# Kernel tuning notes

Measured on AMD Instinct MI355X. Metric: run time of the kernel, lower is better.

## Reference

```python
import math
import jax, jax.numpy as jnp
import numpy as np

B, T, C, H = 1, 512, 768, 12
D = C // H           # head_dim = 64
TOPK_GATE = 128      # config.hoa_top_k
EPS = 1e-5


def _ln(x, w, b):
    m = x.mean(-1, keepdims=True)
    v = ((x - m) ** 2).mean(-1, keepdims=True)
    return (x - m) * jax.lax.rsqrt(v + EPS) * w + b


def _split_heads(x):  # (B,T,C) -> (B,H,T,D)
    return x.reshape(B, T, H, D).transpose(0, 2, 1, 3)


def _sdpa_causal(q, k, v):  # (B,H,T,D) each
    s = jnp.einsum('bhtd,bhsd->bhts', q, k) / math.sqrt(D)
    t = jnp.arange(T)
    s = jnp.where(t[:, None] >= t[None, :], s, -jnp.inf)
    return jnp.einsum('bhts,bhsd->bhtd', jax.nn.softmax(s, axis=-1), v)


def _gather_time(t4, idx):
    # t4: (B,H,T,D), idx: (B,H,T,k) -> (B,H,T,k,D)
    k = idx.shape[-1]
    src = jnp.broadcast_to(t4[:, :, :, None, :], (B, H, T, k, D))
    ind = jnp.broadcast_to(idx[..., None], (B, H, T, k, D))
    return jnp.take_along_axis(src, ind, axis=2)


def _hoa(x, wq, wk1, wk2, wv1, wv2, wo):
    # order-3 higher-order attention with per-branch top-k gathered keys/values
    k_keep = max(1, math.ceil(T ** (2.0 / 3.0)))  # 64 for T=512
    scale = D ** -0.5
    q = _split_heads(x @ wq)
    tar = jnp.arange(T)
    causal_ok = tar[:, None] >= tar[None, :]          # allowed positions
    j = jnp.arange(k_keep)
    # torch code pads short rows (t+1 < k_keep) by repeating the last valid topk idx
    clip = jnp.minimum(j[None, :], tar[:, None])      # (T, k_keep)
    gK, gV = [], []
    for wk, wv in ((wk1, wv1), (wk2, wv2)):
        K = _split_heads(x @ wk)
        V = _split_heads(x @ wv)
        logits = jnp.einsum('bhtd,bhsd->bhts', q, K) * scale
        logits = jnp.where(causal_ok[None, None], logits, -jnp.inf)
        idx = jax.lax.top_k(logits, k_keep)[1]        # (B,H,T,k_keep)
        idx = jnp.take_along_axis(idx, jnp.broadcast_to(clip, idx.shape), axis=-1)
        gK.append(_gather_time(K, idx))
        gV.append(_gather_time(V, idx))
    A = jnp.einsum('bhid,bhijd,bhikd->bhijk', q, gK[0], gK[1]) * scale
    alpha = jax.nn.softmax(A, axis=-1)                # softmax over LAST axis only (as torch)
    out = jnp.einsum('bhijk,bhijd,bhikd->bhid', alpha, gV[0], gV[1])
    return out.transpose(0, 2, 1, 3).reshape(B, T, C) @ wo


def _forward(x, ln1_w, ln1_b, qkv_w, qkv_b, atto_w, atto_b,
             lnh_w, lnh_b, hq_w, hk1_w, hk2_w, hv1_w, hv2_w, ho_w,
             gate_w, gate_b, ln2_w, ln2_b, fc_w, fc_b, pr_w, pr_b):
    # causal self-attention branch
    h = _ln(x, ln1_w, ln1_b)
    qkv = h @ qkv_w + qkv_b
    q, k, v = jnp.split(qkv, 3, axis=-1)
    y = _sdpa_causal(_split_heads(q), _split_heads(k), _split_heads(v))
    y = y.transpose(0, 2, 1, 3).reshape(B, T, C) @ atto_w + atto_b
    x = x + y
    # higher-order attention branch with gated top-k token mask
    hoa_in = _ln(x, lnh_w, lnh_b)
    hoa_out = _hoa(hoa_in, hq_w, hk1_w, hk2_w, hv1_w, hv2_w, ho_w)
    scores = (hoa_in @ gate_w + gate_b)[..., 0]       # (B,T)
    kk = min(TOPK_GATE, T)
    idx = jax.lax.top_k(scores, kk)[1]                # (B,kk)
    mask = jnp.zeros((B, T), x.dtype).at[jnp.arange(B)[:, None], idx].set(1.0)
    x = x + hoa_out * mask[..., None]
    # MLP
    h2 = _ln(x, ln2_w, ln2_b)
    x = x + (jax.nn.gelu(h2 @ fc_w + fc_b, approximate=False) @ pr_w + pr_b)
    return x


def setup_inputs() -> dict:
    key = jax.random.key(0)
    ks = jax.random.split(key, 13)
    def w(k, shape):
        return jax.random.normal(k, shape, jnp.float32) * 0.02
    return dict(
        x=jax.random.normal(ks[0], (B, T, C), jnp.float32),
        ln1_w=jnp.ones(C, jnp.float32), ln1_b=jnp.zeros(C, jnp.float32),
        qkv_w=w(ks[1], (C, 3 * C)), qkv_b=jnp.zeros(3 * C, jnp.float32),
        atto_w=w(ks[2], (C, C)), atto_b=jnp.zeros(C, jnp.float32),
        lnh_w=jnp.ones(C, jnp.float32), lnh_b=jnp.zeros(C, jnp.float32),
        hq_w=w(ks[3], (C, C)), hk1_w=w(ks[4], (C, C)), hk2_w=w(ks[5], (C, C)),
        hv1_w=w(ks[6], (C, C)), hv2_w=w(ks[7], (C, C)), ho_w=w(ks[8], (C, C)),
        gate_w=w(ks[9], (C, 1)), gate_b=jnp.zeros(1, jnp.float32),
        ln2_w=jnp.ones(C, jnp.float32), ln2_b=jnp.zeros(C, jnp.float32),
        fc_w=w(ks[10], (C, 4 * C)), fc_b=jnp.zeros(4 * C, jnp.float32),
        pr_w=w(ks[11], (4 * C, C)), pr_b=jnp.zeros(C, jnp.float32),
    )


def reference(x, ln1_w, ln1_b, qkv_w, qkv_b, atto_w, atto_b,
              lnh_w, lnh_b, hq_w, hk1_w, hk2_w, hv1_w, hv2_w, ho_w,
              gate_w, gate_b, ln2_w, ln2_b, fc_w, fc_b, pr_w, pr_b):
    return _forward(x, ln1_w, ln1_b, qkv_w, qkv_b, atto_w, atto_b,
                    lnh_w, lnh_b, hq_w, hk1_w, hk2_w, hv1_w, hv2_w, ho_w,
                    gate_w, gate_b, ln2_w, ln2_b, fc_w, fc_b, pr_w, pr_b)
```

## Files before the change

kernel.cpp:

```cpp
#include <hip/hip_runtime.h>
#include <hip/hip_bf16.h>
#include <math.h>

#define TT 512
#define CC 768
#define HH 12
#define DD 64
#define KKEEP 64
#define TOPG 128
#define NTCE (TT * CC)
#define NPAIR 36

typedef __attribute__((ext_vector_type(8))) short bf16x8;
typedef __attribute__((ext_vector_type(8))) unsigned short ushort8v;
typedef __attribute__((ext_vector_type(4))) float f32x4;
typedef unsigned long long u64;

__device__ __forceinline__ float block_sum(float v, float* red) {
#pragma unroll
  for (int off = 32; off; off >>= 1) v += __shfl_xor(v, off);
  __syncthreads();
  if ((threadIdx.x & 63) == 0) red[threadIdx.x >> 6] = v;
  __syncthreads();
  return red[0] + red[1] + red[2] + red[3];
}

__device__ __forceinline__ unsigned short f32_to_bf16_rne(float f) {
  unsigned u = __float_as_uint(f);
  unsigned r = (u + 0x7FFFu + ((u >> 16) & 1u)) >> 16;
  return (unsigned short)r;
}
__device__ __forceinline__ float bf16_to_f32(unsigned short h) {
  return __uint_as_float(((unsigned)h) << 16);
}
__device__ __forceinline__ void split2(float x, unsigned short& h, unsigned short& l) {
  h = f32_to_bf16_rne(x);
  l = f32_to_bf16_rne(x - bf16_to_f32(h));
}
__device__ __forceinline__ int swz(int row, int k) {
  return row * 64 + ((((k >> 3) ^ (row & 7))) << 3) + (k & 7);
}

struct WSplitArgs {
  const float* src[10];
  unsigned short* hi[10];
  unsigned short* lo[10];
  int K[10], N[10], tstart[10];
};

__global__ __launch_bounds__(256) void wsplitT_kernel(WSplitArgs a) {
  __shared__ float tile_[64][65];
  int t = blockIdx.x;
  int wsel = 0;
#pragma unroll
  for (int i = 1; i < 10; i++)
    if (t >= a.tstart[i]) wsel = i;
  int local = t - a.tstart[wsel];
  int K = a.K[wsel], N = a.N[wsel];
  int ntn = N >> 6;
  int bn = local % ntn, bk = local / ntn;
  int tid = threadIdx.x, r = tid >> 2, cq = tid & 3;
  const float* src = a.src[wsel] + (size_t)(bk * 64 + r) * N + bn * 64 + cq * 16;
#pragma unroll
  for (int f = 0; f < 4; f++) {
    float4 v = *(const float4*)(src + f * 4);
    tile_[r][cq * 16 + f * 4 + 0] = v.x;
    tile_[r][cq * 16 + f * 4 + 1] = v.y;
    tile_[r][cq * 16 + f * 4 + 2] = v.z;
    tile_[r][cq * 16 + f * 4 + 3] = v.w;
  }
  __syncthreads();
  size_t dst = (size_t)(bn * 64 + r) * K + bk * 64 + cq * 16;
  unsigned short hv[16], lv[16];
#pragma unroll
  for (int i = 0; i < 16; i++) split2(tile_[cq * 16 + i][r], hv[i], lv[i]);
  *(ushort8v*)&a.hi[wsel][dst] = *(const ushort8v*)&hv[0];
  *(ushort8v*)&a.hi[wsel][dst + 8] = *(const ushort8v*)&hv[8];
  *(ushort8v*)&a.lo[wsel][dst] = *(const ushort8v*)&lv[0];
  *(ushort8v*)&a.lo[wsel][dst + 8] = *(const ushort8v*)&lv[8];
}

__global__ void ln_bf_kernel(const float* __restrict__ x, const float* __restrict__ w,
                             const float* __restrict__ b,
                             unsigned short* __restrict__ ohi, unsigned short* __restrict__ olo,
                             const float* __restrict__ gw, const float* __restrict__ gb,
                             float* __restrict__ gscore) {
  int t = blockIdx.x, tid = threadIdx.x;
  __shared__ float red[4];
  float ls = 0.f;
  for (int c = tid; c < CC; c += 256) ls += x[t * CC + c];
  float mean = block_sum(ls, red) * (1.f / CC);
  float lv = 0.f;
  for (int c = tid; c < CC; c += 256) { float d = x[t * CC + c] - mean; lv += d * d; }
  float var = block_sum(lv, red) * (1.f / CC);
  float rs = rsqrtf(var + 1e-5f);
  float gpart = 0.f;
  for (int c = tid; c < CC; c += 256) {
    float val = (x[t * CC + c] - mean) * rs * w[c] + b[c];
    if (gscore) gpart += val * gw[c];
    unsigned short hb, lb;
    split2(val, hb, lb);
    ohi[t * CC + c] = hb;
    olo[t * CC + c] = lb;
  }
  if (gscore) {
    float s = block_sum(gpart, red);
    if (tid == 0) gscore[t] = s + gb[0];
  }
}

__global__ __launch_bounds__(256) void gemm_bf(
    const unsigned short* __restrict__ Ah, const unsigned short* __restrict__ Al,
    const unsigned short* __restrict__ Bh, const unsigned short* __restrict__ Bl,
    const float* __restrict__ bias, float* __restrict__ Cf,
    unsigned short* __restrict__ Chi, unsigned short* __restrict__ Clo,
    int M, int N, int K, int act, int seg, const float* __restrict__ res,
    const float* __restrict__ rowmask, float* __restrict__ part) {
  __shared__ unsigned short AsH[64 * 64], AsL[64 * 64], BsH[64 * 64], BsL[64 * 64];
  int tid = threadIdx.x, lane = tid & 63, wave = tid >> 6;
  int wr = wave >> 1, wc = wave & 1, lr = lane & 15;
  int ksub = (lane >> 4) * 8;
  int n0 = blockIdx.x * 64, m0 = blockIdx.y * 64;
  int lrow = tid >> 2, lq = tid & 3;
  int kchunk = K / gridDim.z;
  int kstart = blockIdx.z * kchunk;

  f32x4 acc[2][2];
#pragma unroll
  for (int i = 0; i < 2; i++)
#pragma unroll
    for (int j = 0; j < 2; j++) acc[i][j] = (f32x4){0.f, 0.f, 0.f, 0.f};

  for (int k0 = kstart; k0 < kstart + kchunk; k0 += 64) {
    size_t aoff = (size_t)(m0 + lrow) * K + k0 + lq * 16;
    size_t boff = (size_t)(n0 + lrow) * K + k0 + lq * 16;
    int d0 = lrow * 64 + (((lq * 2) ^ (lrow & 7)) << 3);
    int d1 = lrow * 64 + (((lq * 2 + 1) ^ (lrow & 7)) << 3);
    *(ushort8v*)&AsH[d0] = *(const ushort8v*)&Ah[aoff];
    *(ushort8v*)&AsH[d1] = *(const ushort8v*)&Ah[aoff + 8];
    *(ushort8v*)&AsL[d0] = *(const ushort8v*)&Al[aoff];
    *(ushort8v*)&AsL[d1] = *(const ushort8v*)&Al[aoff + 8];
    *(ushort8v*)&BsH[d0] = *(const ushort8v*)&Bh[boff];
    *(ushort8v*)&BsH[d1] = *(const ushort8v*)&Bh[boff + 8];
    *(ushort8v*)&BsL[d0] = *(const ushort8v*)&Bl[boff];
    *(ushort8v*)&BsL[d1] = *(const ushort8v*)&Bl[boff + 8];
    __syncthreads();
#pragma unroll
    for (int kb = 0; kb < 2; kb++) {
      int kloc = kb * 32 + ksub;
      bf16x8 ah[2], al[2], bh[2], bl[2];
#pragma unroll
      for (int i = 0; i < 2; i++) {
        int m = wr * 32 + i * 16 + lr;
        int off = swz(m, kloc);
        ah[i] = *(const bf16x8*)&AsH[off];
        al[i] = *(const bf16x8*)&AsL[off];
      }
#pragma unroll
      for (int j = 0; j < 2; j++) {
        int n = wc * 32 + j * 16 + lr;
        int off = swz(n, kloc);
        bh[j] = *(const bf16x8*)&BsH[off];
        bl[j] = *(const bf16x8*)&BsL[off];
      }
#pragma unroll
      for (int i = 0; i < 2; i++)
#pragma unroll
        for (int j = 0; j < 2; j++) {
          acc[i][j] = __builtin_amdgcn_mfma_f32_16x16x32_bf16(ah[i], bh[j], acc[i][j], 0, 0, 0);
          acc[i][j] = __builtin_amdgcn_mfma_f32_16x16x32_bf16(ah[i], bl[j], acc[i][j], 0, 0, 0);
          acc[i][j] = __builtin_amdgcn_mfma_f32_16x16x32_bf16(al[i], bh[j], acc[i][j], 0, 0, 0);
        }
    }
    __syncthreads();
  }
  if (part) {
    float* pb = part + (size_t)blockIdx.z * M * N;
#pragma unroll
    for (int i = 0; i < 2; i++)
#pragma unroll
      for (int j = 0; j < 2; j++) {
        int col = n0 + wc * 32 + j * 16 + lr;
#pragma unroll
        for (int q = 0; q < 4; q++) {
          int row = m0 + wr * 32 + i * 16 + (lane >> 4) * 4 + q;
          pb[(size_t)row * N + col] = acc[i][j][q];
        }
      }
    return;
  }
#pragma unroll
  for (int i = 0; i < 2; i++)
#pragma unroll
    for (int j = 0; j < 2; j++) {
      int col = n0 + wc * 32 + j * 16 + lr;
      float bv = bias ? bias[col] : 0.f;
#pragma unroll
      for (int q = 0; q < 4; q++) {
        int row = m0 + wr * 32 + i * 16 + (lane >> 4) * 4 + q;
        float v = acc[i][j][q] + bv;
        if (act == 1) v = 0.5f * v * (1.f + erff(v * 0.70710678118654752f));
        if (rowmask) v *= rowmask[row];
        if (Cf) {
          size_t off = seg ? (size_t)(col / CC) * NTCE + (size_t)row * CC + (col % CC)
                           : (size_t)row * N + col;
          if (res) v += res[off];
          Cf[off] = v;
        }
        if (Chi) {
          size_t o2 = (size_t)row * N + col;
          unsigned short hb, lb;
          split2(v, hb, lb);
          Chi[o2] = hb;
          Clo[o2] = lb;
        }
      }
    }
}

__global__ __launch_bounds__(256) void gemm_combine_kernel(
    const float* __restrict__ part, int ksplit, int M, int N,
    const float* __restrict__ bias, float* __restrict__ Cf,
    unsigned short* __restrict__ Chi, unsigned short* __restrict__ Clo,
    int act, const float* __restrict__ res, const float* __restrict__ rowmask) {
  int i = blockIdx.x * 256 + threadIdx.x;
  if (i >= M * N) return;
  int row = i / N, col = i - row * N;
  float v = 0.f;
  for (int s = 0; s < ksplit; s++) v += part[(size_t)s * M * N + i];
  if (bias) v += bias[col];
  if (act == 1) v = 0.5f * v * (1.f + erff(v * 0.70710678118654752f));
  if (rowmask) v *= rowmask[row];
  if (Cf) {
    if (res) v += res[i];
    Cf[i] = v;
  }
  if (Chi) {
    unsigned short hb, lb;
    split2(v, hb, lb);
    Chi[i] = hb;
    Clo[i] = lb;
  }
}

__global__ __launch_bounds__(256) void sdpa_part_kernel(
    const float* __restrict__ qkv,
    float* __restrict__ oPart, float* __restrict__ mPart, float* __restrict__ lPart) {
  int h = blockIdx.x;
  int p = blockIdx.y;
  int bt = 0, base = 0;
  while (p >= base + bt + 1) { base += bt + 1; bt++; }
  int st = p - base;
  int t0 = bt * 64, s0 = st * 64;
  int tid = threadIdx.x, lane = tid & 63, w = tid >> 6;
  int lr = lane & 15, ksub = (lane >> 4) * 8;
  const int hDD = h * DD;

  __shared__ unsigned short qHi[64 * 64], qLo[64 * 64];
  __shared__ unsigned short kHi[64 * 64], kLo[64 * 64];
  __shared__ unsigned short bufP[64 * 64], bufV[64 * 64];

  int lrow = tid >> 2, lq = tid & 3;
  {
    const float* srcQ = qkv + (size_t)(t0 + lrow) * (3 * CC) + hDD + lq * 16;
    const float* srcK = qkv + (size_t)(s0 + lrow) * (3 * CC) + CC + hDD + lq * 16;
#pragma unroll
    for (int f = 0; f < 4; f++) {
      float4 v = *(const float4*)(srcQ + f * 4);
      float4 u = *(const float4*)(srcK + f * 4);
      int kk = lq * 16 + f * 4;
      int off = swz(lrow, kk);
      unsigned short h0, h1, h2, h3, l0, l1, l2, l3;
      split2(v.x, h0, l0); split2(v.y, h1, l1); split2(v.z, h2, l2); split2(v.w, h3, l3);
      *(ushort4*)&qHi[off] = make_ushort4(h0, h1, h2, h3);
      *(ushort4*)&qLo[off] = make_ushort4(l0, l1, l2, l3);
      split2(u.x, h0, l0); split2(u.y, h1, l1); split2(u.z, h2, l2); split2(u.w, h3, l3);
      *(ushort4*)&kHi[off] = make_ushort4(h0, h1, h2, h3);
      *(ushort4*)&kLo[off] = make_ushort4(l0, l1, l2, l3);
    }
  }
#pragma unroll
  for (int r = 0; r < 16; r++) {
    int sl = w * 16 + ((r + (lane >> 3)) & 15);
    float v = qkv[(size_t)(s0 + sl) * (3 * CC) + 2 * CC + hDD + lane];
    bufV[swz(lane, sl)] = f32_to_bf16_rne(v);
  }
  __syncthreads();
  f32x4 acc[4];
#pragma unroll
  for (int nt = 0; nt < 4; nt++) acc[nt] = (f32x4){0.f, 0.f, 0.f, 0.f};
  {
    bf16x8 ah[2], al[2];
#pragma unroll
    for (int kb = 0; kb < 2; kb++) {
      int off = swz(w * 16 + lr, kb * 32 + ksub);
      ah[kb] = *(const bf16x8*)&qHi[off];
      al[kb] = *(const bf16x8*)&qLo[off];
    }
#pragma unroll
    for (int nt = 0; nt < 4; nt++)
#pragma unroll
      for (int kb = 0; kb < 2; kb++) {
        int off = swz(nt * 16 + lr, kb * 32 + ksub);
        bf16x8 bh = *(const bf16x8*)&kHi[off];
        bf16x8 bl = *(const bf16x8*)&kLo[off];
        acc[nt] = __builtin_amdgcn_mfma_f32_16x16x32_bf16(ah[kb], bh, acc[nt], 0, 0, 0);
        acc[nt] = __builtin_amdgcn_mfma_f32_16x16x32_bf16(ah[kb], bl, acc[nt], 0, 0, 0);
        acc[nt] = __builtin_amdgcn_mfma_f32_16x16x32_bf16(al[kb], bh, acc[nt], 0, 0, 0);
      }
  }
  int pbase = (h * NPAIR + p) * 64;
#pragma unroll
  for (int q = 0; q < 4; q++) {
    int rloc = w * 16 + (lane >> 4) * 4 + q;
    float tm = -INFINITY;
#pragma unroll
    for (int nt = 0; nt < 4; nt++) {
      float v = acc[nt][q] * 0.125f;
      if (st == bt && nt * 16 + lr > rloc) v = -INFINITY;
      acc[nt][q] = v;
      tm = fmaxf(tm, v);
    }
#pragma unroll
    for (int off = 1; off < 16; off <<= 1) tm = fmaxf(tm, __shfl_xor(tm, off));
    float ps = 0.f;
#pragma unroll
    for (int nt = 0; nt < 4; nt++) {
      float e = __expf(acc[nt][q] - tm);
      acc[nt][q] = e;
      ps += e;
    }
#pragma unroll
    for (int off = 1; off < 16; off <<= 1) ps += __shfl_xor(ps, off);
    if (lr == 0) {
      mPart[pbase + rloc] = tm;
      lPart[pbase + rloc] = ps;
    }
  }
#pragma unroll
  for (int nt = 0; nt < 4; nt++)
#pragma unroll
    for (int q = 0; q < 4; q++) {
      int row = w * 16 + (lane >> 4) * 4 + q;
      int col = nt * 16 + lr;
      bufP[swz(row, col)] = f32_to_bf16_rne(acc[nt][q]);
    }
  __syncthreads();
  f32x4 o[4];
#pragma unroll
  for (int nt = 0; nt < 4; nt++) o[nt] = (f32x4){0.f, 0.f, 0.f, 0.f};
  {
    bf16x8 pf[2];
#pragma unroll
    for (int kb = 0; kb < 2; kb++)
      pf[kb] = *(const bf16x8*)&bufP[swz(w * 16 + lr, kb * 32 + ksub)];
#pragma unroll
    for (int nt = 0; nt < 4; nt++)
#pragma unroll
      for (int kb = 0; kb < 2; kb++) {
        bf16x8 bv = *(const bf16x8*)&bufV[swz(nt * 16 + lr, kb * 32 + ksub)];
        o[nt] = __builtin_amdgcn_mfma_f32_16x16x32_bf16(pf[kb], bv, o[nt], 0, 0, 0);
      }
  }
  float* obase = oPart + ((size_t)(h * NPAIR + p) << 12);
#pragma unroll
  for (int nt = 0; nt < 4; nt++)
#pragma unroll
    for (int q = 0; q < 4; q++) {
      int row = w * 16 + (lane >> 4) * 4 + q;
      int col = nt * 16 + lr;
      obase[row * 64 + col] = o[nt][q];
    }
}

__global__ __launch_bounds__(256) void sdpa_combine_kernel(
    const float* __restrict__ oPart, const float* __restrict__ mPart,
    const float* __restrict__ lPart,
    unsigned short* __restrict__ yhi, unsigned short* __restrict__ ylo) {
  int h = blockIdx.x, bt = blockIdx.y;
  int base = bt * (bt + 1) / 2;
  int n = bt + 1;
  int tid = threadIdx.x;
  int d = tid & 63;
  int r = blockIdx.z * 4 + (tid >> 6);
  int t0 = bt * 64;
  float mg = -INFINITY;
  for (int s = 0; s < n; s++)
    mg = fmaxf(mg, mPart[(h * NPAIR + base + s) * 64 + r]);
  float lg = 0.f, oacc = 0.f;
  for (int s = 0; s < n; s++) {
    int pi = h * NPAIR + base + s;
    float sc = __expf(mPart[pi * 64 + r] - mg);
    lg += sc * lPart[pi * 64 + r];
    oacc += sc * oPart[((size_t)pi << 12) + r * 64 + d];
  }
  float v = oacc / lg;
  unsigned short hb, lb;
  split2(v, hb, lb);
  yhi[(size_t)(t0 + r) * CC + h * DD + d] = hb;
  ylo[(size_t)(t0 + r) * CC + h * DD + d] = lb;
}

__global__ __launch_bounds__(256) void score_gemm_kernel(
    const float* __restrict__ qh, const float* __restrict__ K1, const float* __restrict__ K2,
    float* __restrict__ scores) {
  if (blockIdx.x > blockIdx.y) return;
  int bh = blockIdx.z;
  int br = bh >= HH ? 1 : 0;
  int h = bh - br * HH;
  const float* Kb = br ? K2 : K1;
  int s0 = blockIdx.x * 64, t0 = blockIdx.y * 64;
  int hDD = h * DD;
  __shared__ unsigned short AsH[64 * 64], AsL[64 * 64], BsH[64 * 64], BsL[64 * 64];
  int tid = threadIdx.x, lane = tid & 63, wave = tid >> 6;
  int wr = wave >> 1, wc = wave & 1, lr = lane & 15;
  int ksub = (lane >> 4) * 8;
  int lrow = tid >> 2, lq = tid & 3;
  {
    const float* srcA = qh + (size_t)(t0 + lrow) * CC + hDD + lq * 16;
    const float* srcB = Kb + (size_t)(s0 + lrow) * CC + hDD + lq * 16;
#pragma unroll
    for (int f = 0; f < 4; f++) {
      float4 va = *(const float4*)(srcA + f * 4);
      float4 vb = *(const float4*)(srcB + f * 4);
      int kk = lq * 16 + f * 4;
      int off = swz(lrow, kk);
      unsigned short h0, h1, h2, h3, l0, l1, l2, l3;
      split2(va.x, h0, l0); split2(va.y, h1, l1); split2(va.z, h2, l2); split2(va.w, h3, l3);
      *(ushort4*)&AsH[off] = make_ushort4(h0, h1, h2, h3);
      *(ushort4*)&AsL[off] = make_ushort4(l0, l1, l2, l3);
      split2(vb.x, h0, l0); split2(vb.y, h1, l1); split2(vb.z, h2, l2); split2(vb.w, h3, l3);
      *(ushort4*)&BsH[off] = make_ushort4(h0, h1, h2, h3);
      *(ushort4*)&BsL[off] = make_ushort4(l0, l1, l2, l3);
    }
  }
  __syncthreads();
  f32x4 acc[2][2];
#pragma unroll
  for (int i = 0; i < 2; i++)
#pragma unroll
    for (int j = 0; j < 2; j++) acc[i][j] = (f32x4){0.f, 0.f, 0.f, 0.f};
#pragma unroll
  for (int kb = 0; kb < 2; kb++) {
    int kloc = kb * 32 + ksub;
    bf16x8 ah[2], al[2], bh_[2], bl[2];
#pragma unroll
    for (int i = 0; i < 2; i++) {
      int m = wr * 32 + i * 16 + lr;
      int off = swz(m, kloc);
      ah[i] = *(const bf16x8*)&AsH[off];
      al[i] = *(const bf16x8*)&AsL[off];
    }
#pragma unroll
    for (int j = 0; j < 2; j++) {
      int n = wc * 32 + j * 16 + lr;
      int off = swz(n, kloc);
      bh_[j] = *(const bf16x8*)&BsH[off];
      bl[j] = *(const bf16x8*)&BsL[off];
    }
#pragma unroll
    for (int i = 0; i < 2; i++)
#pragma unroll
      for (int j = 0; j < 2; j++) {
        acc[i][j] = __builtin_amdgcn_mfma_f32_16x16x32_bf16(ah[i], bh_[j], acc[i][j], 0, 0, 0);
        acc[i][j] = __builtin_amdgcn_mfma_f32_16x16x32_bf16(ah[i], bl[j], acc[i][j], 0, 0, 0);
        acc[i][j] = __builtin_amdgcn_mfma_f32_16x16x32_bf16(al[i], bh_[j], acc[i][j], 0, 0, 0);
      }
  }
#pragma unroll
  for (int i = 0; i < 2; i++)
#pragma unroll
    for (int j = 0; j < 2; j++)
#pragma unroll
      for (int q = 0; q < 4; q++) {
        int tt = t0 + wr * 32 + i * 16 + (lane >> 4) * 4 + q;
        int ss = s0 + wc * 32 + j * 16 + lr;
        scores[((size_t)bh * TT + tt) * TT + ss] = acc[i][j][q];
      }
}

template<int CTRL>
__device__ __forceinline__ u64 dpp64(u64 x) {
  unsigned lo = (unsigned)__builtin_amdgcn_update_dpp(
      (int)(unsigned)x, (int)(unsigned)x, CTRL, 0xF, 0xF, true);
  unsigned hi = (unsigned)__builtin_amdgcn_update_dpp(
      (int)(unsigned)(x >> 32), (int)(unsigned)(x >> 32), CTRL, 0xF, 0xF, true);
  return ((u64)hi << 32) | lo;
}
template<int MASK>
__device__ __forceinline__ u64 swz64(u64 x) {
  unsigned lo = (unsigned)__builtin_amdgcn_ds_swizzle((int)(unsigned)x, (MASK << 10) | 0x1F);
  unsigned hi = (unsigned)__builtin_amdgcn_ds_swizzle((int)(unsigned)(x >> 32), (MASK << 10) | 0x1F);
  return ((u64)hi << 32) | lo;
}
__device__ __forceinline__ u64 cas_dir(u64 x, u64 y, bool low) {
  bool take_y = low ? (y > x) : (y < x);
  return take_y ? y : x;
}
__device__ __forceinline__ u64 sort64m(u64 x, int lane) {
  x = cas_dir(x, dpp64<0xB1>(x), (lane & 1) == 0);
  x = cas_dir(x, dpp64<0x1B>(x), (lane & 2) == 0);
  x = cas_dir(x, dpp64<0xB1>(x), (lane & 1) == 0);
  x = cas_dir(x, dpp64<0x141>(x), (lane & 4) == 0);
  x = cas_dir(x, dpp64<0x4E>(x), (lane & 2) == 0);
  x = cas_dir(x, dpp64<0xB1>(x), (lane & 1) == 0);
  x = cas_dir(x, dpp64<0x140>(x), (lane & 8) == 0);
  x = cas_dir(x, swz64<4>(x), (lane & 4) == 0);
  x = cas_dir(x, dpp64<0x4E>(x), (lane & 2) == 0);
  x = cas_dir(x, dpp64<0xB1>(x), (lane & 1) == 0);
  x = cas_dir(x, swz64<31>(x), (lane & 16) == 0);
  x = cas_dir(x, swz64<8>(x), (lane & 8) == 0);
  x = cas_dir(x, swz64<4>(x), (lane & 4) == 0);
  x = cas_dir(x, dpp64<0x4E>(x), (lane & 2) == 0);
  x = cas_dir(x, dpp64<0xB1>(x), (lane & 1) == 0);
  x = cas_dir(x, __shfl_xor(x, 63), (lane & 32) == 0);
  x = cas_dir(x, swz64<16>(x), (lane & 16) == 0);
  x = cas_dir(x, swz64<8>(x), (lane & 8) == 0);
  x = cas_dir(x, swz64<4>(x), (lane & 4) == 0);
  x = cas_dir(x, dpp64<0x4E>(x), (lane & 2) == 0);
  x = cas_dir(x, dpp64<0xB1>(x), (lane & 1) == 0);
  return x;
}
__device__ __forceinline__ u64 merge64m(u64 x, int lane) {
  x = cas_dir(x, __shfl_xor(x, 32), (lane & 32) == 0);
  x = cas_dir(x, swz64<16>(x), (lane & 16) == 0);
  x = cas_dir(x, swz64<8>(x), (lane & 8) == 0);
  x = cas_dir(x, swz64<4>(x), (lane & 4) == 0);
  x = cas_dir(x, dpp64<0x4E>(x), (lane & 2) == 0);
  x = cas_dir(x, dpp64<0xB1>(x), (lane & 1) == 0);
  return x;
}
__device__ __forceinline__ u64 merge2m(u64 a, u64 b, int lane) {
  u64 rev = __shfl_xor(b, 63);
  u64 run = a > rev ? a : rev;
  return merge64m(run, lane);
}
__device__ __forceinline__ u64 make_key(float v, int s, int t) {
  unsigned sv = 0u;
  if (s <= t) {
    unsigned u = __float_as_uint(v);
    sv = (u & 0x80000000u) ? ~u : (u | 0x80000000u);
  }
  return ((u64)sv << 32) | (unsigned)(~s);
}

__global__ __launch_bounds__(256) void topk_select_kernel(
    const float* __restrict__ scores, int* __restrict__ idx1, int* __restrict__ idx2) {
  int tid = threadIdx.x, lane = tid & 63, w = tid >> 6;
  int row = blockIdx.x * 4 + w;
  int br = row >= (HH * TT) ? 1 : 0;
  int rem = row - br * (HH * TT);
  int h = rem >> 9, t = rem & (TT - 1);
  const float* sr = scores + ((size_t)(br * HH + h) * TT + t) * TT;
  int nc = (t >> 6) + 1;
  u64 c[8];
#pragma unroll
  for (int e = 0; e < 8; e++) {
    if (e < nc)
      c[e] = sort64m(make_key(sr[e * 64 + lane], e * 64 + lane, t), lane);
    else
      c[e] = (u64)(unsigned)(~(e * 64 + lane));
  }
  u64 l10 = (t >= 64)  ? merge2m(c[0], c[1], lane) : c[0];
  u64 l11 = (t >= 192) ? merge2m(c[2], c[3], lane) : c[2];
  u64 l12 = (t >= 320) ? merge2m(c[4], c[5], lane) : c[4];
  u64 l13 = (t >= 448) ? merge2m(c[6], c[7], lane) : c[6];
  u64 l20 = (t >= 128) ? merge2m(l10, l11, lane) : l10;
  u64 l21 = (t >= 384) ? merge2m(l12, l13, lane) : l12;
  u64 res = (t >= 256) ? merge2m(l20, l21, lane) : l20;
  unsigned myidx = ~(unsigned)res;
  unsigned outv = __shfl(myidx, min(lane, t));
  int* idxout = (br ? idx2 : idx1) + ((size_t)h * TT + t) * KKEEP;
  idxout[lane] = (int)outv;
}

__device__ __forceinline__ u64 cas_u64(u64 x, int j, bool dirmax, int lane) {
  u64 y = __shfl_xor(x, j);
  bool lower = (lane & j) == 0;
  bool keepmax = (dirmax == lower);
  return (keepmax ? (y > x) : (y < x)) ? y : x;
}
__device__ __forceinline__ void sort512(u64* key, int lane) {
#pragma unroll
  for (int k = 2; k <= 512; k <<= 1) {
#pragma unroll
    for (int j = k >> 1; j > 0; j >>= 1) {
      if (j < 64) {
        bool lower = (lane & j) == 0;
#pragma unroll
        for (int e = 0; e < 8; e++) {
          bool desc = ((((e << 6) | lane) & k) == 0);
          u64 part = __shfl_xor(key[e], j);
          bool wantmax = (desc == lower);
          key[e] = (wantmax ? (part > key[e]) : (part < key[e])) ? part : key[e];
        }
      } else {
        int m = j >> 6;
#pragma unroll
        for (int e = 0; e < 8; e++) {
          if ((e & m) == 0) {
            int e2 = e | m;
            bool desc = ((((e << 6) | lane) & k) == 0);
            u64 a = key[e], b = key[e2];
            u64 mx = a > b ? a : b;
            u64 mn = a > b ? b : a;
            key[e] = desc ? mx : mn;
            key[e2] = desc ? mn : mx;
          }
        }
      }
    }
  }
}

__global__ __launch_bounds__(256) void hoa_core_kernel(
    const float* __restrict__ qh,
    const float* __restrict__ K1, const float* __restrict__ K2,
    const float* __restrict__ V1, const float* __restrict__ V2,
    const int* __restrict__ idx1, const int* __restrict__ idx2,
    unsigned short* __restrict__ hcohi, unsigned short* __restrict__ hcolo) {
  int h = blockIdx.x, t = blockIdx.y, tid = threadIdx.x;
  int lane = tid & 63, w = tid >> 6;
  int lr = lane & 15;
  int ksub = (lane >> 4) * 8;
  const int hDD = h * DD;

  __shared__ unsigned short bufA[64 * 64];
  __shared__ unsigned short bufB[64 * 64];
  __shared__ unsigned short v1s[64 * 68];
  __shared__ float red[4 * 64];
  __shared__ int i1s[64], i2s[64];

  if (tid < 64) {
    i1s[tid] = idx1[(h * TT + t) * KKEEP + tid] * CC + hDD;
    i2s[tid] = idx2[(h * TT + t) * KKEEP + tid] * CC + hDD;
  }
  __syncthreads();

  float qreg = qh[t * CC + hDD + lane];

#pragma unroll
  for (int r = 0; r < 16; r++) {
    int j = w * 16 + r;
    float k1v = K1[i1s[j] + lane];
    float k2v = K2[i2s[j] + lane];
    float v1v = V1[i1s[j] + lane];
    int off = swz(j, lane);
    bufA[off] = f32_to_bf16_rne(k1v * qreg);
    bufB[off] = f32_to_bf16_rne(k2v);
    v1s[j * 68 + lane] = f32_to_bf16_rne(v1v);
  }
  __syncthreads();

  f32x4 acc[4];
#pragma unroll
  for (int nt = 0; nt < 4; nt++) acc[nt] = (f32x4){0.f, 0.f, 0.f, 0.f};
  {
    bf16x8 af[2];
#pragma unroll
    for (int kb = 0; kb < 2; kb++)
      af[kb] = *(const bf16x8*)&bufA[swz(w * 16 + lr, kb * 32 + ksub)];
#pragma unroll
    for (int nt = 0; nt < 4; nt++)
#pragma unroll
      for (int kb = 0; kb < 2; kb++) {
        bf16x8 bf = *(const bf16x8*)&bufB[swz(nt * 16 + lr, kb * 32 + ksub)];
        acc[nt] = __builtin_amdgcn_mfma_f32_16x16x32_bf16(af[kb], bf, acc[nt], 0, 0, 0);
      }
  }
#pragma unroll
  for (int q = 0; q < 4; q++) {
    float m = -INFINITY;
#pragma unroll
    for (int nt = 0; nt < 4; nt++) {
      acc[nt][q] *= 0.125f;
      m = fmaxf(m, acc[nt][q]);
    }
#pragma unroll
    for (int off = 1; off < 16; off <<= 1) m = fmaxf(m, __shfl_xor(m, off));
    float s = 0.f;
#pragma unroll
    for (int nt = 0; nt < 4; nt++) {
      float e = __expf(acc[nt][q] - m);
      acc[nt][q] = e;
      s += e;
    }
#pragma unroll
    for (int off = 1; off < 16; off <<= 1) s += __shfl_xor(s, off);
    float inv = 1.f / s;
#pragma unroll
    for (int nt = 0; nt < 4; nt++) acc[nt][q] *= inv;
  }
  __syncthreads();

#pragma unroll
  for (int nt = 0; nt < 4; nt++)
#pragma unroll
    for (int q = 0; q < 4; q++) {
      int row = w * 16 + (lane >> 4) * 4 + q;
      int col = nt * 16 + lr;
      bufA[swz(row, col)] = f32_to_bf16_rne(acc[nt][q]);
    }
#pragma unroll
  for (int r = 0; r < 16; r++) {
    int kk = w * 16 + ((r + (lane >> 3)) & 15);
    float v2v = V2[i2s[kk] + lane];
    bufB[swz(lane, kk)] = f32_to_bf16_rne(v2v);
  }
  __syncthreads();

  f32x4 acc2[4];
#pragma unroll
  for (int nt = 0; nt < 4; nt++) acc2[nt] = (f32x4){0.f, 0.f, 0.f, 0.f};
  {
    bf16x8 af[2];
#pragma unroll
    for (int kb = 0; kb < 2; kb++)
      af[kb] = *(const bf16x8*)&bufA[swz(w * 16 + lr, kb * 32 + ksub)];
#pragma unroll
    for (int nt = 0; nt < 4; nt++)
#pragma unroll
      for (int kb = 0; kb < 2; kb++) {
        bf16x8 bf = *(const bf16x8*)&bufB[swz(nt * 16 + lr, kb * 32 + ksub)];
        acc2[nt] = __builtin_amdgcn_mfma_f32_16x16x32_bf16(af[kb], bf, acc2[nt], 0, 0, 0);
      }
  }
#pragma unroll
  for (int nt = 0; nt < 4; nt++) {
    float p = 0.f;
#pragma unroll
    for (int q = 0; q < 4; q++) {
      int row = w * 16 + (lane >> 4) * 4 + q;
      int col = lr + 16 * nt;
      p += acc2[nt][q] * bf16_to_f32(v1s[row * 68 + col]);
    }
    p += __shfl_xor(p, 16);
    p += __shfl_xor(p, 32);
    if (lane < 16) red[w * 64 + 16 * nt + lr] = p;
  }
  __syncthreads();
  if (tid < 64) {
    float o = red[tid] + red[64 + tid] + red[128 + tid] + red[192 + tid];
    unsigned short hb, lb;
    split2(o, hb, lb);
    hcohi[t * CC + hDD + tid] = hb;
    hcolo[t * CC + hDD + tid] = lb;
  }
}

__global__ void gate_mask_kernel(const float* __restrict__ scores, float* __restrict__ mask) {
  int lane = threadIdx.x;
  u64 key[8];
#pragma unroll
  for (int e = 0; e < 8; e++) {
    int s = e * 64 + lane;
    unsigned uu = __float_as_uint(scores[s]);
    unsigned sv = (uu & 0x80000000u) ? ~uu : (uu | 0x80000000u);
    key[e] = ((u64)sv << 32) | (unsigned)(~s);
    mask[s] = 0.f;
  }
  __asm__ volatile("s_waitcnt vmcnt(0)" ::: "memory");
  sort512(key, lane);
#pragma unroll
  for (int e = 0; e < 2; e++) mask[(int)(~(unsigned)key[e])] = 1.f;
}

extern "C" void kernel_launch(void* const* d_in, const int* in_sizes, int n_in,
                              void* d_out, int out_size, void* d_ws, size_t ws_size,
                              hipStream_t stream) {
  const float* x      = (const float*)d_in[0];
  const float* ln1_w  = (const float*)d_in[1];
  const float* ln1_b  = (const float*)d_in[2];
  const float* qkv_w  = (const float*)d_in[3];
  const float* qkv_b  = (const float*)d_in[4];
  const float* atto_w = (const float*)d_in[5];
  const float* atto_b = (const float*)d_in[6];
  const float* lnh_w  = (const float*)d_in[7];
  const float* lnh_b  = (const float*)d_in[8];
  const float* hq_w   = (const float*)d_in[9];
  const float* hk1_w  = (const float*)d_in[10];
  const float* hk2_w  = (const float*)d_in[11];
  const float* hv1_w  = (const float*)d_in[12];
  const float* hv2_w  = (const float*)d_in[13];
  const float* ho_w   = (const float*)d_in[14];
  const float* gate_w = (const float*)d_in[15];
  const float* gate_b = (const float*)d_in[16];
  const float* ln2_w  = (const float*)d_in[17];
  const float* ln2_b  = (const float*)d_in[18];
  const float* fc_w   = (const float*)d_in[19];
  const float* fc_b   = (const float*)d_in[20];
  const float* pr_w   = (const float*)d_in[21];
  const float* pr_b   = (const float*)d_in[22];
  float* out = (float*)d_out;

  char* cur = (char*)d_ws;
  auto alloc = [&](size_t bytes) {
    char* p = cur;
    cur += (bytes + 255) & ~(size_t)255;
    return p;
  };
  float* qkv  = (float*)alloc((size_t)3 * NTCE * 4);
  float* x1   = (float*)alloc((size_t)NTCE * 4);
  float* qh   = (float*)alloc((size_t)5 * NTCE * 4);
  float* K1   = qh + NTCE;
  float* K2   = K1 + NTCE;
  float* V1   = K2 + NTCE;
  float* V2   = V1 + NTCE;
  float* x2   = (float*)alloc((size_t)NTCE * 4);
  float* scores = (float*)alloc(TT * 4);
  float* maskb  = (float*)alloc(TT * 4);
  int* idx1 = (int*)alloc((size_t)HH * TT * KKEEP * 4);
  int* idx2 = (int*)alloc((size_t)HH * TT * KKEEP * 4);
  float* hscores = (float*)alloc((size_t)2 * HH * TT * TT * 4);
  float* oPart = (float*)alloc((size_t)HH * NPAIR * 64 * 64 * 4);
  float* mPart = (float*)alloc((size_t)HH * NPAIR * 64 * 4);
  float* lPart = (float*)alloc((size_t)HH * NPAIR * 64 * 4);
  float* gpart = (float*)alloc((size_t)2 * TT * 4 * CC * 4);
  unsigned short* hHi    = (unsigned short*)alloc((size_t)NTCE * 2);
  unsigned short* hLo    = (unsigned short*)alloc((size_t)NTCE * 2);
  unsigned short* yHi    = (unsigned short*)alloc((size_t)NTCE * 2);
  unsigned short* yLo    = (unsigned short*)alloc((size_t)NTCE * 2);
  unsigned short* hoinHi = (unsigned short*)alloc((size_t)NTCE * 2);
  unsigned short* hoinLo = (unsigned short*)alloc((size_t)NTCE * 2);
  unsigned short* h2Hi   = (unsigned short*)alloc((size_t)NTCE * 2);
  unsigned short* h2Lo   = (unsigned short*)alloc((size_t)NTCE * 2);
  unsigned short* hcoHi  = (unsigned short*)alloc((size_t)NTCE * 2);
  unsigned short* hcoLo  = (unsigned short*)alloc((size_t)NTCE * 2);
  unsigned short* fcbHi  = (unsigned short*)alloc((size_t)4 * NTCE * 2);
  unsigned short* fcbLo  = (unsigned short*)alloc((size_t)4 * NTCE * 2);
  const size_t WSQ = (size_t)CC * CC;
  unsigned short* qkvT_h = (unsigned short*)alloc((size_t)CC * 3 * CC * 2);
  unsigned short* qkvT_l = (unsigned short*)alloc((size_t)CC * 3 * CC * 2);
  unsigned short* attoT_h = (unsigned short*)alloc(WSQ * 2);
  unsigned short* attoT_l = (unsigned short*)alloc(WSQ * 2);
  unsigned short* hoaT_h = (unsigned short*)alloc(5 * WSQ * 2);
  unsigned short* hoaT_l = (unsigned short*)alloc(5 * WSQ * 2);
  unsigned short* hoT_h = (unsigned short*)alloc(WSQ * 2);
  unsigned short* hoT_l = (unsigned short*)alloc(WSQ * 2);
  unsigned short* fcT_h = (unsigned short*)alloc((size_t)CC * 4 * CC * 2);
  unsigned short* fcT_l = (unsigned short*)alloc((size_t)CC * 4 * CC * 2);
  unsigned short* prT_h = (unsigned short*)alloc((size_t)CC * 4 * CC * 2);
  unsigned short* prT_l = (unsigned short*)alloc((size_t)CC * 4 * CC * 2);

  WSplitArgs wa;
  int tcur = 0;
  auto addw = [&](int i, const float* s, unsigned short* hi, unsigned short* lo, int K, int N) {
    wa.src[i] = s; wa.hi[i] = hi; wa.lo[i] = lo;
    wa.K[i] = K; wa.N[i] = N; wa.tstart[i] = tcur;
    tcur += (N / 64) * (K / 64);
  };
  addw(0, qkv_w, qkvT_h, qkvT_l, CC, 3 * CC);
  addw(1, atto_w, attoT_h, attoT_l, CC, CC);
  addw(2, hq_w,  hoaT_h + 0 * WSQ, hoaT_l + 0 * WSQ, CC, CC);
  addw(3, hk1_w, hoaT_h + 1 * WSQ, hoaT_l + 1 * WSQ, CC, CC);
  addw(4, hk2_w, hoaT_h + 2 * WSQ, hoaT_l + 2 * WSQ, CC, CC);
  addw(5, hv1_w, hoaT_h + 3 * WSQ, hoaT_l + 3 * WSQ, CC, CC);
  addw(6, hv2_w, hoaT_h + 4 * WSQ, hoaT_l + 4 * WSQ, CC, CC);
  addw(7, ho_w, hoT_h, hoT_l, CC, CC);
  addw(8, fc_w, fcT_h, fcT_l, CC, 4 * CC);
  addw(9, pr_w, prT_h, prT_l, 4 * CC, CC);

  dim3 blk(256);
  const float* nullf = nullptr;

  hipLaunchKernelGGL(wsplitT_kernel, dim3(tcur), blk, 0, stream, wa);
  hipLaunchKernelGGL(ln_bf_kernel, dim3(TT), blk, 0, stream, x, ln1_w, ln1_b,
                     hHi, hLo, nullf, nullf, (float*)nullptr);
  hipLaunchKernelGGL(gemm_bf, dim3(36, 8, 2), blk, 0, stream, hHi, hLo, qkvT_h, qkvT_l,
                     nullf, (float*)nullptr, (unsigned short*)nullptr, (unsigned short*)nullptr,
                     TT, 3 * CC, CC, 0, 0, nullf, nullf, gpart);
  hipLaunchKernelGGL(gemm_combine_kernel, dim3((TT * 3 * CC + 255) / 256), blk, 0, stream,
                     gpart, 2, TT, 3 * CC, qkv_b, qkv,
                     (unsigned short*)nullptr, (unsigned short*)nullptr, 0, nullf, nullf);
  hipLaunchKernelGGL(sdpa_part_kernel, dim3(HH, NPAIR), blk, 0, stream,
                     qkv, oPart, mPart, lPart);
  hipLaunchKernelGGL(sdpa_combine_kernel, dim3(HH, 8, 16), blk, 0, stream,
                     oPart, mPart, lPart, yHi, yLo);
  hipLaunchKernelGGL(gemm_bf, dim3(12, 8, 2), blk, 0, stream, yHi, yLo, attoT_h, attoT_l,
                     nullf, (float*)nullptr, (unsigned short*)nullptr, (unsigned short*)nullptr,
                     TT, CC, CC, 0, 0, nullf, nullf, gpart);
  hipLaunchKernelGGL(gemm_combine_kernel, dim3((NTCE + 255) / 256), blk, 0, stream,
                     gpart, 2, TT, CC, atto_b, x1,
                     (unsigned short*)nullptr, (unsigned short*)nullptr, 0, x, nullf);
  hipLaunchKernelGGL(ln_bf_kernel, dim3(TT), blk, 0, stream, x1, lnh_w, lnh_b,
                     hoinHi, hoinLo, gate_w, gate_b, scores);
  hipLaunchKernelGGL(gate_mask_kernel, dim3(1), dim3(64), 0, stream, scores, maskb);
  hipLaunchKernelGGL(gemm_bf, dim3(60, 8, 1), blk, 0, stream, hoinHi, hoinLo, hoaT_h, hoaT_l,
                     nullf, qh, (unsigned short*)nullptr, (unsigned short*)nullptr,
                     TT, 5 * CC, CC, 0, 1, nullf, nullf, (float*)nullptr);
  hipLaunchKernelGGL(score_gemm_kernel, dim3(8, 8, 2 * HH), blk, 0, stream,
                     qh, K1, K2, hscores);
  hipLaunchKernelGGL(topk_select_kernel, dim3(2 * HH * TT / 4), blk, 0, stream,
                     hscores, idx1, idx2);
  hipLaunchKernelGGL(hoa_core_kernel, dim3(HH, TT), blk, 0, stream,
                     qh, K1, K2, V1, V2, idx1, idx2, hcoHi, hcoLo);
  hipLaunchKernelGGL(gemm_bf, dim3(12, 8, 2), blk, 0, stream, hcoHi, hcoLo, hoT_h, hoT_l,
                     nullf, (float*)nullptr, (unsigned short*)nullptr, (unsigned short*)nullptr,
                     TT, CC, CC, 0, 0, nullf, nullf, gpart);
  hipLaunchKernelGGL(gemm_combine_kernel, dim3((NTCE + 255) / 256), blk, 0, stream,
                     gpart, 2, TT, CC, nullf, x2,
                     (unsigned short*)nullptr, (unsigned short*)nullptr, 0, x1, maskb);
  hipLaunchKernelGGL(ln_bf_kernel, dim3(TT), blk, 0, stream, x2, ln2_w, ln2_b,
                     h2Hi, h2Lo, nullf, nullf, (float*)nullptr);
  hipLaunchKernelGGL(gemm_bf, dim3(48, 8, 2), blk, 0, stream, h2Hi, h2Lo, fcT_h, fcT_l,
                     nullf, (float*)nullptr, (unsigned short*)nullptr, (unsigned short*)nullptr,
                     TT, 4 * CC, CC, 1, 0, nullf, nullf, gpart);
  hipLaunchKernelGGL(gemm_combine_kernel, dim3((TT * 4 * CC + 255) / 256), blk, 0, stream,
                     gpart, 2, TT, 4 * CC, fc_b, (float*)nullptr,
                     fcbHi, fcbLo, 1, nullf, nullf);
  hipLaunchKernelGGL(gemm_bf, dim3(12, 8, 4), blk, 0, stream, fcbHi, fcbLo, prT_h, prT_l,
                     nullf, (float*)nullptr, (unsigned short*)nullptr, (unsigned short*)nullptr,
                     TT, CC, 4 * CC, 0, 0, nullf, nullf, gpart);
  hipLaunchKernelGGL(gemm_combine_kernel, dim3((NTCE + 255) / 256), blk, 0, stream,
                     gpart, 4, TT, CC, pr_b, out,
                     (unsigned short*)nullptr, (unsigned short*)nullptr, 0, x2, nullf);
}
```

Before: 256.4 us.

## Emit HOA projections as packed bf16 hi/lo pairs and consume them directly

The 5-way HOA projection GEMM now writes bf16 hi/lo split outputs in a row-interleaved (T, 5C) layout instead of separate fp32 q/K1/K2/V1/V2 head-major buffers. The score GEMM loads pre-split bf16 tiles with 16-byte vector copies instead of converting fp32 in the kernel, and the HOA core gathers bf16 K/V rows directly. This halves gather bytes and removes repeated float-to-bf16 conversion work. The trade-off is that the HOA core's K1 values now use only the hi half before multiplying by q, whereas before it used the full fp32 value before rounding, which slightly changes precision.

```diff
diff --git a/kernel.cpp b/kernel.cpp
--- a/kernel.cpp
+++ b/kernel.cpp
@@ -10,6 +10,7 @@
 #define TOPG 128
 #define NTCE (TT * CC)
 #define NPAIR 36
+#define PW (5 * CC)
 
 typedef __attribute__((ext_vector_type(8))) short bf16x8;
 typedef __attribute__((ext_vector_type(8))) unsigned short ushort8v;
@@ -402,37 +403,33 @@
 }
 
 __global__ __launch_bounds__(256) void score_gemm_kernel(
-    const float* __restrict__ qh, const float* __restrict__ K1, const float* __restrict__ K2,
+    const unsigned short* __restrict__ ph, const unsigned short* __restrict__ pl,
     float* __restrict__ scores) {
   if (blockIdx.x > blockIdx.y) return;
   int bh = blockIdx.z;
   int br = bh >= HH ? 1 : 0;
   int h = bh - br * HH;
-  const float* Kb = br ? K2 : K1;
   int s0 = blockIdx.x * 64, t0 = blockIdx.y * 64;
   int hDD = h * DD;
+  int kcol = (1 + br) * CC + hDD;
   __shared__ unsigned short AsH[64 * 64], AsL[64 * 64], BsH[64 * 64], BsL[64 * 64];
   int tid = threadIdx.x, lane = tid & 63, wave = tid >> 6;
   int wr = wave >> 1, wc = wave & 1, lr = lane & 15;
   int ksub = (lane >> 4) * 8;
   int lrow = tid >> 2, lq = tid & 3;
   {
-    const float* srcA = qh + (size_t)(t0 + lrow) * CC + hDD + lq * 16;
-    const float* srcB = Kb + (size_t)(s0 + lrow) * CC + hDD + lq * 16;
-#pragma unroll
-    for (int f = 0; f < 4; f++) {
-      float4 va = *(const float4*)(srcA + f * 4);
-      float4 vb = *(const float4*)(srcB + f * 4);
-      int kk = lq * 16 + f * 4;
-      int off = swz(lrow, kk);
-      unsigned short h0, h1, h2, h3, l0, l1, l2, l3;
-      split2(va.x, h0, l0); split2(va.y, h1, l1); split2(va.z, h2, l2); split2(va.w, h3, l3);
-      *(ushort4*)&AsH[off] = make_ushort4(h0, h1, h2, h3);
-      *(ushort4*)&AsL[off] = make_ushort4(l0, l1, l2, l3);
-      split2(vb.x, h0, l0); split2(vb.y, h1, l1); split2(vb.z, h2, l2); split2(vb.w, h3, l3);
-      *(ushort4*)&BsH[off] = make_ushort4(h0, h1, h2, h3);
-      *(ushort4*)&BsL[off] = make_ushort4(l0, l1, l2, l3);
-    }
+    size_t aoff = (size_t)(t0 + lrow) * PW + hDD + lq * 16;
+    size_t boff = (size_t)(s0 + lrow) * PW + kcol + lq * 16;
+    int d0 = lrow * 64 + (((lq * 2) ^ (lrow & 7)) << 3);
+    int d1 = lrow * 64 + (((lq * 2 + 1) ^ (lrow & 7)) << 3);
+    *(ushort8v*)&AsH[d0] = *(const ushort8v*)&ph[aoff];
+    *(ushort8v*)&AsH[d1] = *(const ushort8v*)&ph[aoff + 8];
+    *(ushort8v*)&AsL[d0] = *(const ushort8v*)&pl[aoff];
+    *(ushort8v*)&AsL[d1] = *(const ushort8v*)&pl[aoff + 8];
+    *(ushort8v*)&BsH[d0] = *(const ushort8v*)&ph[boff];
+    *(ushort8v*)&BsH[d1] = *(const ushort8v*)&ph[boff + 8];
+    *(ushort8v*)&BsL[d0] = *(const ushort8v*)&pl[boff];
+    *(ushort8v*)&BsL[d1] = *(const ushort8v*)&pl[boff + 8];
   }
   __syncthreads();
   f32x4 acc[2][2];
@@ -614,9 +611,7 @@
 }
 
 __global__ __launch_bounds__(256) void hoa_core_kernel(
-    const float* __restrict__ qh,
-    const float* __restrict__ K1, const float* __restrict__ K2,
-    const float* __restrict__ V1, const float* __restrict__ V2,
+    const unsigned short* __restrict__ ph, const unsigned short* __restrict__ pl,
     const int* __restrict__ idx1, const int* __restrict__ idx2,
     unsigned short* __restrict__ hcohi, unsigned short* __restrict__ hcolo) {
   int h = blockIdx.x, t = blockIdx.y, tid = threadIdx.x;
@@ -632,23 +627,22 @@
   __shared__ int i1s[64], i2s[64];
 
   if (tid < 64) {
-    i1s[tid] = idx1[(h * TT + t) * KKEEP + tid] * CC + hDD;
-    i2s[tid] = idx2[(h * TT + t) * KKEEP + tid] * CC + hDD;
-  }
-  __syncthreads();
-
-  float qreg = qh[t * CC + hDD + lane];
+    i1s[tid] = idx1[(h * TT + t) * KKEEP + tid] * PW + CC + hDD;
+    i2s[tid] = idx2[(h * TT + t) * KKEEP + tid] * PW + 2 * CC + hDD;
+  }
+  __syncthreads();
+
+  size_t qoff = (size_t)t * PW + hDD + lane;
+  float qreg = bf16_to_f32(ph[qoff]) + bf16_to_f32(pl[qoff]);
 
 #pragma unroll
   for (int r = 0; r < 16; r++) {
     int j = w * 16 + r;
-    float k1v = K1[i1s[j] + lane];
-    float k2v = K2[i2s[j] + lane];
-    float v1v = V1[i1s[j] + lane];
+    float k1v = bf16_to_f32(ph[i1s[j] + lane]);
     int off = swz(j, lane);
     bufA[off] = f32_to_bf16_rne(k1v * qreg);
-    bufB[off] = f32_to_bf16_rne(k2v);
-    v1s[j * 68 + lane] = f32_to_bf16_rne(v1v);
+    bufB[off] = ph[i2s[j] + lane];
+    v1s[j * 68 + lane] = ph[i1s[j] + 2 * CC + lane];
   }
   __syncthreads();
 
@@ -704,8 +698,7 @@
 #pragma unroll
   for (int r = 0; r < 16; r++) {
     int kk = w * 16 + ((r + (lane >> 3)) & 15);
-    float v2v = V2[i2s[kk] + lane];
-    bufB[swz(lane, kk)] = f32_to_bf16_rne(v2v);
+    bufB[swz(lane, kk)] = ph[i2s[kk] + 2 * CC + lane];
   }
   __syncthreads();
 
@@ -801,11 +794,6 @@
   };
   float* qkv  = (float*)alloc((size_t)3 * NTCE * 4);
   float* x1   = (float*)alloc((size_t)NTCE * 4);
-  float* qh   = (float*)alloc((size_t)5 * NTCE * 4);
-  float* K1   = qh + NTCE;
-  float* K2   = K1 + NTCE;
-  float* V1   = K2 + NTCE;
-  float* V2   = V1 + NTCE;
   float* x2   = (float*)alloc((size_t)NTCE * 4);
   float* scores = (float*)alloc(TT * 4);
   float* maskb  = (float*)alloc(TT * 4);
@@ -822,6 +810,8 @@
   unsigned short* yLo    = (unsigned short*)alloc((size_t)NTCE * 2);
   unsigned short* hoinHi = (unsigned short*)alloc((size_t)NTCE * 2);
   unsigned short* hoinLo = (unsigned short*)alloc((size_t)NTCE * 2);
+  unsigned short* hoaPh  = (unsigned short*)alloc((size_t)TT * PW * 2);
+  unsigned short* hoaPl  = (unsigned short*)alloc((size_t)TT * PW * 2);
   unsigned short* h2Hi   = (unsigned short*)alloc((size_t)NTCE * 2);
   unsigned short* h2Lo   = (unsigned short*)alloc((size_t)NTCE * 2);
   unsigned short* hcoHi  = (unsigned short*)alloc((size_t)NTCE * 2);
@@ -886,14 +876,14 @@
                      hoinHi, hoinLo, gate_w, gate_b, scores);
   hipLaunchKernelGGL(gate_mask_kernel, dim3(1), dim3(64), 0, stream, scores, maskb);
   hipLaunchKernelGGL(gemm_bf, dim3(60, 8, 1), blk, 0, stream, hoinHi, hoinLo, hoaT_h, hoaT_l,
-                     nullf, qh, (unsigned short*)nullptr, (unsigned short*)nullptr,
-                     TT, 5 * CC, CC, 0, 1, nullf, nullf, (float*)nullptr);
+                     nullf, (float*)nullptr, hoaPh, hoaPl,
+                     TT, PW, CC, 0, 0, nullf, nullf, (float*)nullptr);
   hipLaunchKernelGGL(score_gemm_kernel, dim3(8, 8, 2 * HH), blk, 0, stream,
-                     qh, K1, K2, hscores);
+                     hoaPh, hoaPl, hscores);
   hipLaunchKernelGGL(topk_select_kernel, dim3(2 * HH * TT / 4), blk, 0, stream,
                      hscores, idx1, idx2);
   hipLaunchKernelGGL(hoa_core_kernel, dim3(HH, TT), blk, 0, stream,
-                     qh, K1, K2, V1, V2, idx1, idx2, hcoHi, hcoLo);
+                     hoaPh, hoaPl, idx1, idx2, hcoHi, hcoLo);
   hipLaunchKernelGGL(gemm_bf, dim3(12, 8, 2), blk, 0, stream, hcoHi, hcoLo, hoT_h, hoT_l,
                      nullf, (float*)nullptr, (unsigned short*)nullptr, (unsigned short*)nullptr,
                      TT, CC, CC, 0, 0, nullf, nullf, gpart);
```

Measured after the change: 252.7 us. About the same (-1.5%).
